# Kernel optimization log

Measured on AMD Instinct MI355X. Metric: run time of the kernel, lower is better.

## Reference

```python
import jax, jax.numpy as jnp
import numpy as np

N = 8192      # total nodes
B = 64        # graphs in batch
NPG = 128     # nodes per graph (equal-size graphs; idx sorted)
D_IN = 256
H = 256       # hidden_dim (d_model)
NH = 4        # nhead
HD = H // NH
FF = 2 * H    # dim_feedforward
NC = 16       # n_class


def setup_inputs() -> dict:
    key = jax.random.key(0)
    ks = jax.random.split(key, 16)
    def rn(k, shp, scale=0.05):
        return jax.random.normal(k, shp, jnp.float32) * scale
    inp = {}
    inp["x_in"] = jax.random.normal(ks[0], (N, D_IN), jnp.float32)
    # scale adjacency so each row sums ~1 to keep activations well-conditioned
    inp["adj"] = jax.random.uniform(ks[1], (N, N), jnp.float32) * (2.0 / N)
    inp["idx"] = jnp.repeat(jnp.arange(B, dtype=jnp.int32), NPG)
    inp["cum_nodes"] = jnp.full((B,), NPG, jnp.int32)
    # fc1
    inp["W1"] = rn(ks[2], (D_IN, H)); inp["b1"] = jnp.zeros((H,), jnp.float32)
    # transformer encoder layer (eval mode, dropout inactive)
    inp["in_w"] = rn(ks[3], (H, 3 * H)); inp["in_b"] = jnp.zeros((3 * H,), jnp.float32)
    inp["out_w"] = rn(ks[4], (H, H));    inp["out_b"] = jnp.zeros((H,), jnp.float32)
    inp["ln1_s"] = jnp.ones((H,), jnp.float32); inp["ln1_b"] = jnp.zeros((H,), jnp.float32)
    inp["ff1_w"] = rn(ks[5], (H, FF)); inp["ff1_b"] = jnp.zeros((FF,), jnp.float32)
    inp["ff2_w"] = rn(ks[6], (FF, H)); inp["ff2_b"] = jnp.zeros((H,), jnp.float32)
    inp["ln2_s"] = jnp.ones((H,), jnp.float32); inp["ln2_b"] = jnp.zeros((H,), jnp.float32)
    # fc3 / fc4
    inp["W3"] = rn(ks[7], (H, H));  inp["b3"] = jnp.zeros((H,), jnp.float32)
    inp["W4"] = rn(ks[8], (H, NC)); inp["b4"] = jnp.zeros((NC,), jnp.float32)
    return inp


def _layer_norm(x, s, b):
    mu = x.mean(-1, keepdims=True)
    xc = x - mu
    return xc * jax.lax.rsqrt((xc * xc).mean(-1, keepdims=True) + 1e-5) * s + b


def reference(x_in, adj, idx, cum_nodes, W1, b1, in_w, in_b, out_w, out_b,
              ln1_s, ln1_b, ff1_w, ff1_b, ff2_w, ff2_b, ln2_s, ln2_b,
              W3, b3, W4, b4):
    Bg = cum_nodes.shape[0]
    n = x_in.shape[0] // Bg  # equal-size graphs -> pad_sequence == reshape
    x = x_in @ W1 + b1                      # fc1
    x = jax.nn.relu(adj @ x)                # adjacency message passing
    p = x.reshape(Bg, n, H)                 # pack: idx is sorted, graphs equal size
    # --- TransformerEncoderLayer (post-LN, relu FFN, eval mode) ---
    qkv = p @ in_w + in_b                   # [B, n, 3H]
    q, k, v = jnp.split(qkv, 3, axis=-1)
    q = q.reshape(Bg, n, NH, HD); k = k.reshape(Bg, n, NH, HD); v = v.reshape(Bg, n, NH, HD)
    att = jax.nn.softmax(jnp.einsum('bqhd,bkhd->bhqk', q, k) / np.sqrt(HD), axis=-1)
    o = jnp.einsum('bhqk,bkhd->bqhd', att, v).reshape(Bg, n, H) @ out_w + out_b
    y = _layer_norm(p + o, ln1_s, ln1_b)
    ff = jax.nn.relu(y @ ff1_w + ff1_b) @ ff2_w + ff2_b
    y = _layer_norm(y + ff, ln2_s, ln2_b)
    # --- unpack + scatter-add pooling over graphs ---
    flat = y.reshape(Bg * n, H)
    pooled = jax.ops.segment_sum(flat, idx, num_segments=Bg)  # [B, H]
    out = jax.nn.relu(pooled @ W3 + b3) @ W4 + b4
    return jax.nn.log_softmax(out, axis=-1)
```

## Files before the change

kernel.cpp:

```cpp
#include <hip/hip_runtime.h>

typedef float fx4 __attribute__((ext_vector_type(4)));
typedef short s16x8 __attribute__((ext_vector_type(8)));
typedef short s16x4 __attribute__((ext_vector_type(4)));
typedef unsigned short ushort_t;

__device__ __forceinline__ short f2bf(float f) {
  union { float f; unsigned u; } v; v.f = f;
  unsigned r = v.u + 0x7FFFu + ((v.u >> 16) & 1u);
  return (short)(r >> 16);
}

__device__ __forceinline__ float bf2f(short h) {
  union { float f; unsigned u; } v;
  v.u = ((unsigned)(unsigned short)h) << 16;
  return v.f;
}

__device__ __forceinline__ unsigned cvt_pk_bf16(float a, float b) {
  unsigned r;
  asm("v_cvt_pk_bf16_f32 %0, %1, %2" : "=v"(r) : "v"(a), "v"(b));
  return r;
}

__device__ __forceinline__ s16x8 cvt8(fx4 a, fx4 b) {
  union { s16x8 s; unsigned u[4]; } w;
  w.u[0] = cvt_pk_bf16(a[0], a[1]);
  w.u[1] = cvt_pk_bf16(a[2], a[3]);
  w.u[2] = cvt_pk_bf16(b[0], b[1]);
  w.u[3] = cvt_pk_bf16(b[2], b[3]);
  return w.s;
}

__device__ __forceinline__ void gload16(const void* g, void* l) {
  __builtin_amdgcn_global_load_lds(
      (const __attribute__((address_space(1))) unsigned int*)g,
      (__attribute__((address_space(3))) unsigned int*)l, 16, 0, 0);
}

__global__ __launch_bounds__(256) void prep_kernel(
    const float* __restrict__ W1, const float* __restrict__ in_w,
    const float* __restrict__ out_w, const float* __restrict__ ff1_w,
    const float* __restrict__ ff2_w,
    ushort_t* __restrict__ W1t, ushort_t* __restrict__ in_wT,
    ushort_t* __restrict__ out_wT, ushort_t* __restrict__ ff1t,
    ushort_t* __restrict__ ff2t) {
  const int bid = blockIdx.x, t = threadIdx.x;
  const float* W; ushort_t* Wt; int K, N, base;
  if (bid < 256)       { W = W1;    Wt = W1t;    K = 256; N = 256; base = 0; }
  else if (bid < 1024) { W = in_w;  Wt = in_wT;  K = 256; N = 768; base = 256; }
  else if (bid < 1280) { W = out_w; Wt = out_wT; K = 256; N = 256; base = 1024; }
  else if (bid < 1792) { W = ff1_w; Wt = ff1t;   K = 256; N = 512; base = 1280; }
  else                 { W = ff2_w; Wt = ff2t;   K = 512; N = 256; base = 1792; }
  const int idx = (bid - base) * 256 + t;
  const int k = idx / N, n = idx - k * N;
  Wt[(size_t)n * K + k] = (ushort_t)f2bf(W[idx]);
}

template<int MF, bool AF32, int OUTM, bool RELU, bool RES>
__global__ __launch_bounds__(256) void gemm2(
    const void* __restrict__ Av, const ushort_t* __restrict__ Bt,
    const float* __restrict__ bias, const float* __restrict__ res,
    const float* __restrict__ lns, const float* __restrict__ lnb,
    float* __restrict__ Cf, ushort_t* __restrict__ Cb,
    int M, int N, int K, int kLen) {
  constexpr int BM = MF * 16;
  __shared__ __align__(16) ushort_t Asm[2][BM * 64];
  __shared__ __align__(16) ushort_t Bsm[256 * 64];
  const int t = threadIdx.x, lane = t & 63, wave = t >> 6;
  const int bm = blockIdx.y * BM;
  const int bn = blockIdx.x * 256;
  const int wn = wave * 64, fr = lane & 15, fq = lane >> 4;
  const int NT = kLen >> 6;
  const int x0 = ((fq) ^ (fr & 7)) * 8;
  const int x1 = ((4 + fq) ^ (fr & 7)) * 8;
  fx4 acc[MF][4] = {};

  const int gl = lane >> 3, gc = lane & 7;
  const int gsw = (gc ^ gl) * 8;
  const ushort_t* Bgl = Bt + (size_t)(bn + wave * 64 + gl) * K + gsw;
  const ushort_t* Agl =
      (const ushort_t*)Av + (size_t)(bm + wave * (BM / 4) + gl) * K + gsw;
  constexpr int TPR = 256 / BM;
  const int arow = t / TPR;
  const int ac0 = (t % TPR) * (BM / 4);
  const float* Afp = (const float*)Av + (size_t)(bm + arow) * K + ac0;
  fx4 R[MF / 2][2];

  auto issueB = [&](int kt) {
    #pragma unroll
    for (int i = 0; i < 8; ++i)
      gload16(Bgl + (size_t)i * 8 * K + kt * 64, &Bsm[wave * 4096 + i * 512]);
  };
  auto issueAg = [&](int buf, int kt) {
    #pragma unroll
    for (int i = 0; i < MF / 2; ++i)
      gload16(Agl + (size_t)i * 8 * K + kt * 64,
              &Asm[buf][wave * (BM * 16) + i * 512]);
  };
  auto loadR = [&](int kt) {
    #pragma unroll
    for (int w = 0; w < MF / 2; ++w) {
      R[w][0] = *(const fx4*)(Afp + kt * 64 + w * 8);
      R[w][1] = *(const fx4*)(Afp + kt * 64 + w * 8 + 4);
    }
  };
  auto writeA = [&](int buf) {
    #pragma unroll
    for (int w = 0; w < MF / 2; ++w) {
      const int cs = ((ac0 >> 3) + w) ^ (arow & 7);
      *(s16x8*)&Asm[buf][arow * 64 + cs * 8] = cvt8(R[w][0], R[w][1]);
    }
  };

  if constexpr (AF32) { loadR(0); issueB(0); writeA(0); loadR(1); }
  else { issueAg(0, 0); issueB(0); }
  __syncthreads();

  #pragma unroll 1
  for (int kt = 0; kt < NT; ++kt) {
    const int cur = kt & 1;
    s16x8 b0[4], b1[4], a0[MF], a1[MF];
    #pragma unroll
    for (int nf = 0; nf < 4; ++nf) {
      b0[nf] = *(const s16x8*)&Bsm[(wn + nf * 16 + fr) * 64 + x0];
      b1[nf] = *(const s16x8*)&Bsm[(wn + nf * 16 + fr) * 64 + x1];
    }
    #pragma unroll
    for (int mf = 0; mf < MF; ++mf)
      a0[mf] = *(const s16x8*)&Asm[cur][(mf * 16 + fr) * 64 + x0];
    asm volatile("s_waitcnt lgkmcnt(0)" ::: "memory");
    if (kt + 1 < NT) {
      if constexpr (AF32) {
        writeA(cur ^ 1);
        if (kt + 2 < NT) loadR(kt + 2);
        issueB(kt + 1);
      } else {
        issueAg(cur ^ 1, kt + 1);
        issueB(kt + 1);
      }
    }
    #pragma unroll
    for (int mf = 0; mf < MF; ++mf)
      #pragma unroll
      for (int nf = 0; nf < 4; ++nf)
        acc[mf][nf] = __builtin_amdgcn_mfma_f32_16x16x32_bf16(
            a0[mf], b0[nf], acc[mf][nf], 0, 0, 0);
    #pragma unroll
    for (int mf = 0; mf < MF; ++mf)
      a1[mf] = *(const s16x8*)&Asm[cur][(mf * 16 + fr) * 64 + x1];
    #pragma unroll
    for (int mf = 0; mf < MF; ++mf)
      #pragma unroll
      for (int nf = 0; nf < 4; ++nf)
        acc[mf][nf] = __builtin_amdgcn_mfma_f32_16x16x32_bf16(
            a1[mf], b1[nf], acc[mf][nf], 0, 0, 0);
    __syncthreads();
  }

  if constexpr (OUTM == 3) {
    #pragma unroll
    for (int mf = 0; mf < MF; ++mf)
      #pragma unroll
      for (int nf = 0; nf < 4; ++nf) {
        const int col = bn + wn + nf * 16 + fr;
        const float bb = bias[col];
        s16x4 w;
        #pragma unroll
        for (int r = 0; r < 4; ++r) w[r] = f2bf(acc[mf][nf][r] + bb);
        *(s16x4*)&Cb[(size_t)col * M + bm + mf * 16 + fq * 4] = w;
      }
  } else {
    #pragma unroll
    for (int mf = 0; mf < MF; ++mf)
      #pragma unroll
      for (int nf = 0; nf < 4; ++nf) {
        const int col = bn + wn + nf * 16 + fr;
        const float bb = bias[col];
        #pragma unroll
        for (int r = 0; r < 4; ++r) {
          const int row = bm + mf * 16 + fq * 4 + r;
          float x = acc[mf][nf][r] + bb;
          if constexpr (RES) x += res[(size_t)row * N + col];
          if constexpr (RELU) x = fmaxf(x, 0.f);
          if constexpr (OUTM == 0 || OUTM == 2) Cf[(size_t)row * N + col] = x;
          if constexpr (OUTM == 1 || OUTM == 2)
            Cb[(size_t)row * N + col] = (ushort_t)f2bf(x);
        }
      }
  }
}

__global__ __launch_bounds__(256) void adjmm2(
    const float* __restrict__ adj, const ushort_t* __restrict__ xT,
    ushort_t* __restrict__ part) {
  constexpr int NT = 32;
  __shared__ __align__(16) ushort_t Asm[2][64 * 64];
  __shared__ __align__(16) ushort_t Bsm[2][256 * 64];
  const int t = threadIdx.x, lane = t & 63, wave = t >> 6;
  const int kh = blockIdx.x, bm = blockIdx.y * 64;
  const int kOff = kh * 2048;
  const int wn = wave * 64, fr = lane & 15, fq = lane >> 4;
  const int x0 = (fq ^ (fr & 7)) * 8, x1 = ((4 + fq) ^ (fr & 7)) * 8;
  const int gl = lane >> 3, gc = lane & 7, gsw = (gc ^ gl) * 8;

  const ushort_t* Bgl = xT + (size_t)(wn + gl) * 8192 + kOff + gsw;
  const int arow = t >> 2;
  const int ac0 = (t & 3) * 16;
  const float* Afp = adj + (size_t)(bm + arow) * 8192 + kOff + ac0;

  fx4 R[2][2];
  auto loadR = [&](int kt) {
    #pragma unroll
    for (int w = 0; w < 2; ++w) {
      R[w][0] = *(const fx4*)(Afp + kt * 64 + w * 8);
      R[w][1] = *(const fx4*)(Afp + kt * 64 + w * 8 + 4);
    }
  };
  auto writeA = [&](int buf) {
    #pragma unroll
    for (int w = 0; w < 2; ++w) {
      const int cs = ((ac0 >> 3) + w) ^ (arow & 7);
      *(s16x8*)&Asm[buf][arow * 64 + cs * 8] = cvt8(R[w][0], R[w][1]);
    }
  };
  auto issueB = [&](int buf, int kt) {
    #pragma unroll
    for (int i = 0; i < 8; ++i)
      gload16(Bgl + (size_t)i * 8 * 8192 + kt * 64,
              &Bsm[buf][wave * 4096 + i * 512]);
  };

  fx4 acc[4][4] = {};
  loadR(0);
  issueB(0, 0);
  writeA(0);
  loadR(1);
  asm volatile("s_waitcnt lgkmcnt(0)" ::: "memory");
  asm volatile("s_waitcnt vmcnt(4)" ::: "memory");
  __builtin_amdgcn_sched_barrier(0);
  __builtin_amdgcn_s_barrier();
  __builtin_amdgcn_sched_barrier(0);
  issueB(1, 1);

  #pragma unroll 1
  for (int kt = 0; kt < NT; ++kt) {
    const int cur = kt & 1;
    s16x8 a0[4], a1[4], b0[4], b1[4];
    #pragma unroll
    for (int mf = 0; mf < 4; ++mf) {
      a0[mf] = *(const s16x8*)&Asm[cur][(mf * 16 + fr) * 64 + x0];
      a1[mf] = *(const s16x8*)&Asm[cur][(mf * 16 + fr) * 64 + x1];
    }
    #pragma unroll
    for (int nf = 0; nf < 4; ++nf) {
      b0[nf] = *(const s16x8*)&Bsm[cur][(wn + nf * 16 + fr) * 64 + x0];
      b1[nf] = *(const s16x8*)&Bsm[cur][(wn + nf * 16 + fr) * 64 + x1];
    }
    if (kt + 1 < NT) {
      writeA(cur ^ 1);
      if (kt + 2 < NT) loadR(kt + 2);
    }
    #pragma unroll
    for (int mf = 0; mf < 4; ++mf)
      #pragma unroll
      for (int nf = 0; nf < 4; ++nf)
        acc[mf][nf] = __builtin_amdgcn_mfma_f32_16x16x32_bf16(
            a0[mf], b0[nf], acc[mf][nf], 0, 0, 0);
    #pragma unroll
    for (int mf = 0; mf < 4; ++mf)
      #pragma unroll
      for (int nf = 0; nf < 4; ++nf)
        acc[mf][nf] = __builtin_amdgcn_mfma_f32_16x16x32_bf16(
            a1[mf], b1[nf], acc[mf][nf], 0, 0, 0);
    asm volatile("s_waitcnt lgkmcnt(0)" ::: "memory");
    if (kt + 2 < NT)
      asm volatile("s_waitcnt vmcnt(4)" ::: "memory");
    else
      asm volatile("s_waitcnt vmcnt(0)" ::: "memory");
    __builtin_amdgcn_sched_barrier(0);
    __builtin_amdgcn_s_barrier();
    __builtin_amdgcn_sched_barrier(0);
    if (kt + 2 < NT) issueB(cur, kt + 2);
  }

  ushort_t* po = part + (size_t)kh * (8192ull * 256ull);
  #pragma unroll
  for (int mf = 0; mf < 4; ++mf)
    #pragma unroll
    for (int nf = 0; nf < 4; ++nf)
      #pragma unroll
      for (int r = 0; r < 4; ++r)
        po[(size_t)(bm + mf * 16 + fq * 4 + r) * 256 + wn + nf * 16 + fr] =
            (ushort_t)f2bf(acc[mf][nf][r]);
}

__global__ __launch_bounds__(256) void relu_reduce4(
    const ushort_t* __restrict__ part, float* __restrict__ p,
    ushort_t* __restrict__ pb) {
  const size_t i = ((size_t)blockIdx.x * 256 + threadIdx.x) * 8;
  const size_t S = 8192ull * 256ull;
  float a[8] = {};
  #pragma unroll
  for (int j = 0; j < 4; ++j) {
    const s16x8 v = *(const s16x8*)(part + j * S + i);
    #pragma unroll
    for (int c = 0; c < 8; ++c) a[c] += bf2f(v[c]);
  }
  fx4 v0, v1;
  #pragma unroll
  for (int c = 0; c < 4; ++c) {
    v0[c] = fmaxf(a[c], 0.f);
    v1[c] = fmaxf(a[c + 4], 0.f);
  }
  *(fx4*)(p + i) = v0;
  *(fx4*)(p + i + 4) = v1;
  s16x8 w;
  #pragma unroll
  for (int c = 0; c < 4; ++c) { w[c] = f2bf(v0[c]); w[c + 4] = f2bf(v1[c]); }
  *(s16x8*)(pb + i) = w;
}

__global__ __launch_bounds__(256) void att_fused(
    const ushort_t* __restrict__ qkv, ushort_t* __restrict__ attout) {
  __shared__ float k_s[128][68];
  __shared__ float v_s[128][68];
  __shared__ float s_s[128][129];
  __shared__ float pm[2][128];
  __shared__ float ps[2][128];
  const int bh = blockIdx.x, b = bh >> 2, h = bh & 3;
  const int t = threadIdx.x;
  const ushort_t* qb = qkv + (size_t)b * 128 * 768 + h * 64;
  for (int u = t; u < 1024; u += 256) {
    const int n = u >> 3, d8 = (u & 7) * 8;
    const s16x8 kk = *(const s16x8*)(qb + (size_t)n * 768 + 256 + d8);
    const s16x8 vv = *(const s16x8*)(qb + (size_t)n * 768 + 512 + d8);
    #pragma unroll
    for (int c = 0; c < 8; ++c) {
      k_s[n][d8 + c] = bf2f(kk[c]);
      v_s[n][d8 + c] = bf2f(vv[c]);
    }
  }
  const int row = t & 127, kh = t >> 7;
  fx4 qr[16];
  {
    const s16x8* q8 = (const s16x8*)(qb + (size_t)row * 768);
    #pragma unroll
    for (int j = 0; j < 8; ++j) {
      const s16x8 qv = q8[j];
      qr[2*j][0] = bf2f(qv[0]); qr[2*j][1] = bf2f(qv[1]);
      qr[2*j][2] = bf2f(qv[2]); qr[2*j][3] = bf2f(qv[3]);
      qr[2*j+1][0] = bf2f(qv[4]); qr[2*j+1][1] = bf2f(qv[5]);
      qr[2*j+1][2] = bf2f(qv[6]); qr[2*j+1][3] = bf2f(qv[7]);
    }
  }
  __syncthreads();
  float m = -1e30f;
  for (int j = 0; j < 64; ++j) {
    const int jj = kh * 64 + j;
    const fx4* kr = (const fx4*)&k_s[jj][0];
    float s0 = 0.f, s1 = 0.f, s2 = 0.f, s3 = 0.f;
    #pragma unroll
    for (int c = 0; c < 16; c += 4) {
      fx4 k0 = kr[c], k1 = kr[c + 1], k2 = kr[c + 2], k3 = kr[c + 3];
      s0 += qr[c][0]*k0[0] + qr[c][1]*k0[1] + qr[c][2]*k0[2] + qr[c][3]*k0[3];
      s1 += qr[c+1][0]*k1[0] + qr[c+1][1]*k1[1] + qr[c+1][2]*k1[2] + qr[c+1][3]*k1[3];
      s2 += qr[c+2][0]*k2[0] + qr[c+2][1]*k2[1] + qr[c+2][2]*k2[2] + qr[c+2][3]*k2[3];
      s3 += qr[c+3][0]*k3[0] + qr[c+3][1]*k3[1] + qr[c+3][2]*k3[2] + qr[c+3][3]*k3[3];
    }
    const float s = (s0 + s1 + s2 + s3) * 0.125f;
    s_s[row][jj] = s;
    m = fmaxf(m, s);
  }
  pm[kh][row] = m;
  __syncthreads();
  const float m2 = fmaxf(pm[0][row], pm[1][row]);
  float sum = 0.f;
  for (int j = 0; j < 64; ++j) {
    const int jj = kh * 64 + j;
    const float e = __expf(s_s[row][jj] - m2);
    s_s[row][jj] = e;
    sum += e;
  }
  ps[kh][row] = sum;
  __syncthreads();
  const int row2 = t >> 1, dh = (t & 1) * 32;
  const float inv = 1.f / (ps[0][row2] + ps[1][row2]);
  fx4 acc4[8] = {};
  for (int k = 0; k < 128; ++k) {
    const float e = s_s[row2][k];
    const fx4* vr = (const fx4*)&v_s[k][dh];
    #pragma unroll
    for (int c = 0; c < 8; ++c) acc4[c] += e * vr[c];
  }
  ushort_t* orow = attout + (size_t)(b * 128 + row2) * 256 + h * 64 + dh;
  #pragma unroll
  for (int c = 0; c < 8; ++c) {
    const fx4 v = acc4[c] * inv;
    s16x4 w;
    #pragma unroll
    for (int j = 0; j < 4; ++j) w[j] = f2bf(v[j]);
    *(s16x4*)(orow + c * 4) = w;
  }
}

__global__ __launch_bounds__(256) void tail_kernel(
    const ushort_t* __restrict__ attout, const ushort_t* __restrict__ out_wT,
    const float* __restrict__ out_b, const float* __restrict__ p_res,
    const float* __restrict__ ln1_s, const float* __restrict__ ln1_b,
    const ushort_t* __restrict__ ff1t, const float* __restrict__ ff1_b,
    const ushort_t* __restrict__ ff2t, const float* __restrict__ ff2_b,
    const float* __restrict__ ln2_s, const float* __restrict__ ln2_b,
    float* __restrict__ pooled4) {
  __shared__ __align__(16) ushort_t Asm[2][32 * 64];
  __shared__ __align__(16) ushort_t Bsm[256 * 64];
  __shared__ __align__(16) ushort_t y_s[32 * 256];
  __shared__ __align__(16) ushort_t f1_s[32 * 512];
  __shared__ float red_s[128], red_q[128];
  const int t = threadIdx.x, lane = t & 63, wave = t >> 6;
  const int bq = blockIdx.x, bm = bq * 32;
  const int wn = wave * 64, fr = lane & 15, fq = lane >> 4;
  const int x0 = (fq ^ (fr & 7)) * 8, x1 = ((4 + fq) ^ (fr & 7)) * 8;
  const int gl = lane >> 3, gc = lane & 7, gsw = (gc ^ gl) * 8;

  fx4 acc[2][4] = {};
  {
    const ushort_t* Agl = attout + (size_t)(bm + wave * 8 + gl) * 256 + gsw;
    const ushort_t* Bgl = out_wT + (size_t)(wave * 64 + gl) * 256 + gsw;
    auto issueA = [&](int buf, int kt) {
      gload16(Agl + kt * 64, &Asm[buf][wave * 512]);
    };
    auto issueB = [&](int kt) {
      #pragma unroll
      for (int i = 0; i < 8; ++i)
        gload16(Bgl + (size_t)i * 8 * 256 + kt * 64,
                &Bsm[wave * 4096 + i * 512]);
    };
    issueA(0, 0); issueB(0);
    __syncthreads();
    #pragma unroll 1
    for (int kt = 0; kt < 4; ++kt) {
      const int cur = kt & 1;
      s16x8 b0[4], b1[4], a0[2], a1[2];
      #pragma unroll
      for (int nf = 0; nf < 4; ++nf) {
        b0[nf] = *(const s16x8*)&Bsm[(wn + nf * 16 + fr) * 64 + x0];
        b1[nf] = *(const s16x8*)&Bsm[(wn + nf * 16 + fr) * 64 + x1];
      }
      #pragma unroll
      for (int mf = 0; mf < 2; ++mf) {
        a0[mf] = *(const s16x8*)&Asm[cur][(mf * 16 + fr) * 64 + x0];
        a1[mf] = *(const s16x8*)&Asm[cur][(mf * 16 + fr) * 64 + x1];
      }
      asm volatile("s_waitcnt lgkmcnt(0)" ::: "memory");
      if (kt < 3) { issueA(cur ^ 1, kt + 1); issueB(kt + 1); }
      #pragma unroll
      for (int mf = 0; mf < 2; ++mf)
        #pragma unroll
        for (int nf = 0; nf < 4; ++nf) {
          acc[mf][nf] = __builtin_amdgcn_mfma_f32_16x16x32_bf16(
              a0[mf], b0[nf], acc[mf][nf], 0, 0, 0);
          acc[mf][nf] = __builtin_amdgcn_mfma_f32_16x16x32_bf16(
              a1[mf], b1[nf], acc[mf][nf], 0, 0, 0);
        }
      __syncthreads();
    }
  }
  float yv[2][4][4];
  #pragma unroll
  for (int mf = 0; mf < 2; ++mf)
    #pragma unroll
    for (int nf = 0; nf < 4; ++nf) {
      const int col = wn + nf * 16 + fr;
      #pragma unroll
      for (int r = 0; r < 4; ++r) {
        const int row = bm + mf * 16 + fq * 4 + r;
        yv[mf][nf][r] = acc[mf][nf][r] + out_b[col] +
                        p_res[(size_t)row * 256 + col];
      }
    }
  {
    #pragma unroll
    for (int mf = 0; mf < 2; ++mf)
      #pragma unroll
      for (int r = 0; r < 4; ++r) {
        float s = yv[mf][0][r] + yv[mf][1][r] + yv[mf][2][r] + yv[mf][3][r];
        float q = yv[mf][0][r]*yv[mf][0][r] + yv[mf][1][r]*yv[mf][1][r] +
                  yv[mf][2][r]*yv[mf][2][r] + yv[mf][3][r]*yv[mf][3][r];
        #pragma unroll
        for (int off = 1; off < 16; off <<= 1) {
          s += __shfl_xor(s, off, 64);
          q += __shfl_xor(q, off, 64);
        }
        if (fr == 0) {
          red_s[(mf * 16 + fq * 4 + r) * 4 + wave] = s;
          red_q[(mf * 16 + fq * 4 + r) * 4 + wave] = q;
        }
      }
    __syncthreads();
    #pragma unroll
    for (int mf = 0; mf < 2; ++mf)
      #pragma unroll
      for (int r = 0; r < 4; ++r) {
        const int rl = mf * 16 + fq * 4 + r;
        const float st = red_s[rl*4] + red_s[rl*4+1] + red_s[rl*4+2] + red_s[rl*4+3];
        const float qt = red_q[rl*4] + red_q[rl*4+1] + red_q[rl*4+2] + red_q[rl*4+3];
        const float mu = st * (1.f / 256.f);
        const float rr = rsqrtf(qt * (1.f / 256.f) - mu * mu + 1e-5f);
        #pragma unroll
        for (int nf = 0; nf < 4; ++nf) {
          const int col = wn + nf * 16 + fr;
          const float o = (yv[mf][nf][r] - mu) * rr * ln1_s[col] + ln1_b[col];
          yv[mf][nf][r] = o;
          y_s[rl * 256 + ((col >> 3) ^ (rl & 7)) * 8 + (col & 7)] =
              (ushort_t)f2bf(o);
        }
      }
  }
  __syncthreads();

  #pragma unroll 1
  for (int ng = 0; ng < 2; ++ng) {
    const ushort_t* Bgl = ff1t + (size_t)(ng * 256 + wave * 64 + gl) * 256 + gsw;
    auto issueB = [&](int kt) {
      #pragma unroll
      for (int i = 0; i < 8; ++i)
        gload16(Bgl + (size_t)i * 8 * 256 + kt * 64,
                &Bsm[wave * 4096 + i * 512]);
    };
    fx4 a2[2][4] = {};
    issueB(0);
    #pragma unroll 1
    for (int kt = 0; kt < 4; ++kt) {
      asm volatile("s_waitcnt vmcnt(0)" ::: "memory");
      s16x8 b0[4], b1[4], a0[2], a1[2];
      #pragma unroll
      for (int nf = 0; nf < 4; ++nf) {
        b0[nf] = *(const s16x8*)&Bsm[(wn + nf * 16 + fr) * 64 + x0];
        b1[nf] = *(const s16x8*)&Bsm[(wn + nf * 16 + fr) * 64 + x1];
      }
      #pragma unroll
      for (int mf = 0; mf < 2; ++mf) {
        const int row = mf * 16 + fr;
        a0[mf] = *(const s16x8*)&y_s[row * 256 + ((kt*8 + fq) ^ (row & 7)) * 8];
        a1[mf] = *(const s16x8*)&y_s[row * 256 + ((kt*8 + 4 + fq) ^ (row & 7)) * 8];
      }
      asm volatile("s_waitcnt lgkmcnt(0)" ::: "memory");
      if (kt < 3) issueB(kt + 1);
      #pragma unroll
      for (int mf = 0; mf < 2; ++mf)
        #pragma unroll
        for (int nf = 0; nf < 4; ++nf) {
          a2[mf][nf] = __builtin_amdgcn_mfma_f32_16x16x32_bf16(
              a0[mf], b0[nf], a2[mf][nf], 0, 0, 0);
          a2[mf][nf] = __builtin_amdgcn_mfma_f32_16x16x32_bf16(
              a1[mf], b1[nf], a2[mf][nf], 0, 0, 0);
        }
    }
    #pragma unroll
    for (int mf = 0; mf < 2; ++mf)
      #pragma unroll
      for (int nf = 0; nf < 4; ++nf) {
        const int col = ng * 256 + wn + nf * 16 + fr;
        const float bb = ff1_b[col];
        #pragma unroll
        for (int r = 0; r < 4; ++r) {
          const int rl = mf * 16 + fq * 4 + r;
          const float x = fmaxf(a2[mf][nf][r] + bb, 0.f);
          f1_s[rl * 512 + ((col >> 3) ^ (rl & 7)) * 8 + (col & 7)] =
              (ushort_t)f2bf(x);
        }
      }
  }
  __syncthreads();

  {
    const ushort_t* Bgl = ff2t + (size_t)(wave * 64 + gl) * 512 + gsw;
    auto issueB = [&](int kt) {
      #pragma unroll
      for (int i = 0; i < 8; ++i)
        gload16(Bgl + (size_t)i * 8 * 512 + kt * 64,
                &Bsm[wave * 4096 + i * 512]);
    };
    fx4 a3[2][4] = {};
    issueB(0);
    #pragma unroll 1
    for (int kt = 0; kt < 8; ++kt) {
      asm volatile("s_waitcnt vmcnt(0)" ::: "memory");
      s16x8 b0[4], b1[4], a0[2], a1[2];
      #pragma unroll
      for (int nf = 0; nf < 4; ++nf) {
        b0[nf] = *(const s16x8*)&Bsm[(wn + nf * 16 + fr) * 64 + x0];
        b1[nf] = *(const s16x8*)&Bsm[(wn + nf * 16 + fr) * 64 + x1];
      }
      #pragma unroll
      for (int mf = 0; mf < 2; ++mf) {
        const int row = mf * 16 + fr;
        a0[mf] = *(const s16x8*)&f1_s[row * 512 + ((kt*8 + fq) ^ (row & 7)) * 8];
        a1[mf] = *(const s16x8*)&f1_s[row * 512 + ((kt*8 + 4 + fq) ^ (row & 7)) * 8];
      }
      asm volatile("s_waitcnt lgkmcnt(0)" ::: "memory");
      if (kt < 7) issueB(kt + 1);
      #pragma unroll
      for (int mf = 0; mf < 2; ++mf)
        #pragma unroll
        for (int nf = 0; nf < 4; ++nf) {
          a3[mf][nf] = __builtin_amdgcn_mfma_f32_16x16x32_bf16(
              a0[mf], b0[nf], a3[mf][nf], 0, 0, 0);
          a3[mf][nf] = __builtin_amdgcn_mfma_f32_16x16x32_bf16(
              a1[mf], b1[nf], a3[mf][nf], 0, 0, 0);
        }
    }
    float vv[2][4][4];
    #pragma unroll
    for (int mf = 0; mf < 2; ++mf)
      #pragma unroll
      for (int nf = 0; nf < 4; ++nf) {
        const int col = wn + nf * 16 + fr;
        const float bb = ff2_b[col];
        #pragma unroll
        for (int r = 0; r < 4; ++r)
          vv[mf][nf][r] = a3[mf][nf][r] + bb + yv[mf][nf][r];
      }
    __syncthreads();
    #pragma unroll
    for (int mf = 0; mf < 2; ++mf)
      #pragma unroll
      for (int r = 0; r < 4; ++r) {
        float s = vv[mf][0][r] + vv[mf][1][r] + vv[mf][2][r] + vv[mf][3][r];
        float q = vv[mf][0][r]*vv[mf][0][r] + vv[mf][1][r]*vv[mf][1][r] +
                  vv[mf][2][r]*vv[mf][2][r] + vv[mf][3][r]*vv[mf][3][r];
        #pragma unroll
        for (int off = 1; off < 16; off <<= 1) {
          s += __shfl_xor(s, off, 64);
          q += __shfl_xor(q, off, 64);
        }
        if (fr == 0) {
          red_s[(mf * 16 + fq * 4 + r) * 4 + wave] = s;
          red_q[(mf * 16 + fq * 4 + r) * 4 + wave] = q;
        }
      }
    __syncthreads();
    float colsum[4] = {};
    #pragma unroll
    for (int mf = 0; mf < 2; ++mf)
      #pragma unroll
      for (int r = 0; r < 4; ++r) {
        const int rl = mf * 16 + fq * 4 + r;
        const float st = red_s[rl*4] + red_s[rl*4+1] + red_s[rl*4+2] + red_s[rl*4+3];
        const float qt = red_q[rl*4] + red_q[rl*4+1] + red_q[rl*4+2] + red_q[rl*4+3];
        const float mu = st * (1.f / 256.f);
        const float rr = rsqrtf(qt * (1.f / 256.f) - mu * mu + 1e-5f);
        #pragma unroll
        for (int nf = 0; nf < 4; ++nf) {
          const int col = wn + nf * 16 + fr;
          colsum[nf] += (vv[mf][nf][r] - mu) * rr * ln2_s[col] + ln2_b[col];
        }
      }
    #pragma unroll
    for (int nf = 0; nf < 4; ++nf) {
      colsum[nf] += __shfl_xor(colsum[nf], 16, 64);
      colsum[nf] += __shfl_xor(colsum[nf], 32, 64);
    }
    if (lane < 16)
      #pragma unroll
      for (int nf = 0; nf < 4; ++nf)
        pooled4[(size_t)bq * 256 + wn + nf * 16 + fr] = colsum[nf];
  }
}

__global__ __launch_bounds__(256) void head_kernel(
    const float* __restrict__ pooled4, const float* __restrict__ W3,
    const float* __restrict__ b3, const float* __restrict__ W4,
    const float* __restrict__ b4, float* __restrict__ out) {
  __shared__ float sp[256];
  __shared__ float t1[256];
  __shared__ float logits[16];
  const int b = blockIdx.x, h = threadIdx.x;
  sp[h] = pooled4[(size_t)(b * 4 + 0) * 256 + h] +
          pooled4[(size_t)(b * 4 + 1) * 256 + h] +
          pooled4[(size_t)(b * 4 + 2) * 256 + h] +
          pooled4[(size_t)(b * 4 + 3) * 256 + h];
  __syncthreads();
  float a = b3[h];
  for (int k = 0; k < 256; ++k) a += sp[k] * W3[k * 256 + h];
  t1[h] = fmaxf(a, 0.f);
  __syncthreads();
  if (h < 16) {
    float o = b4[h];
    for (int j = 0; j < 256; ++j) o += t1[j] * W4[j * 16 + h];
    logits[h] = o;
  }
  __syncthreads();
  if (h < 16) {
    float mm = -1e30f;
    #pragma unroll
    for (int c = 0; c < 16; ++c) mm = fmaxf(mm, logits[c]);
    float se = 0.f;
    #pragma unroll
    for (int c = 0; c < 16; ++c) se += __expf(logits[c] - mm);
    out[b * 16 + h] = logits[h] - mm - logf(se);
  }
}

extern "C" void kernel_launch(void* const* d_in, const int* in_sizes, int n_in,
                              void* d_out, int out_size, void* d_ws, size_t ws_size,
                              hipStream_t stream) {
  const float* x_in  = (const float*)d_in[0];
  const float* adj   = (const float*)d_in[1];
  const float* W1    = (const float*)d_in[4];
  const float* b1    = (const float*)d_in[5];
  const float* in_w  = (const float*)d_in[6];
  const float* in_b  = (const float*)d_in[7];
  const float* out_w = (const float*)d_in[8];
  const float* out_b = (const float*)d_in[9];
  const float* ln1_s = (const float*)d_in[10];
  const float* ln1_b = (const float*)d_in[11];
  const float* ff1_w = (const float*)d_in[12];
  const float* ff1_b = (const float*)d_in[13];
  const float* ff2_w = (const float*)d_in[14];
  const float* ff2_b = (const float*)d_in[15];
  const float* ln2_s = (const float*)d_in[16];
  const float* ln2_b = (const float*)d_in[17];
  const float* W3    = (const float*)d_in[18];
  const float* b3    = (const float*)d_in[19];
  const float* W4    = (const float*)d_in[20];
  const float* b4    = (const float*)d_in[21];
  char* ws = (char*)d_ws;
  const size_t MB = 1ull << 20;
  ushort_t* xT      = (ushort_t*)(ws);
  ushort_t* W1t     = (ushort_t*)(ws + 4 * MB);
  ushort_t* in_wT   = (ushort_t*)(ws + 4 * MB + 131072);
  ushort_t* out_wT  = (ushort_t*)(ws + 4 * MB + 524288);
  ushort_t* ff1t    = (ushort_t*)(ws + 4 * MB + 655360);
  ushort_t* ff2t    = (ushort_t*)(ws + 4 * MB + 917504);
  float*    p       = (float*)(ws + 8 * MB);
  ushort_t* p_bf    = (ushort_t*)(ws + 16 * MB);
  ushort_t* qkv_bf  = (ushort_t*)(ws + 20 * MB);
  ushort_t* attout  = (ushort_t*)(ws + 32 * MB);
  float*    pooled4 = (float*)(ws + 36 * MB);
  ushort_t* part    = (ushort_t*)(ws + 37 * MB);
  float*    outp    = (float*)d_out;
  (void)in_sizes; (void)n_in; (void)out_size; (void)ws_size;

  prep_kernel<<<2304, 256, 0, stream>>>(W1, in_w, out_w, ff1_w, ff2_w,
                                        W1t, in_wT, out_wT, ff1t, ff2t);
  gemm2<2, true, 3, false, false><<<dim3(1, 256), 256, 0, stream>>>(
      x_in, W1t, b1, nullptr, nullptr, nullptr, nullptr, xT,
      8192, 256, 256, 256);
  adjmm2<<<dim3(4, 128), 256, 0, stream>>>(adj, xT, part);
  relu_reduce4<<<1024, 256, 0, stream>>>(part, p, p_bf);
  gemm2<4, false, 1, false, false><<<dim3(3, 128), 256, 0, stream>>>(
      p_bf, in_wT, in_b, nullptr, nullptr, nullptr, nullptr, qkv_bf,
      8192, 768, 256, 256);
  att_fused<<<256, 256, 0, stream>>>(qkv_bf, attout);
  tail_kernel<<<256, 256, 0, stream>>>(
      attout, out_wT, out_b, p, ln1_s, ln1_b, ff1t, ff1_b,
      ff2t, ff2_b, ln2_s, ln2_b, pooled4);
  head_kernel<<<64, 256, 0, stream>>>(pooled4, W3, b3, W4, b4, outp);
}
```

Before: 183.3 us.

## Load adjacency tiles straight into MFMA fragment registers, drop A LDS staging

The adjacency GEMM kernel now has each wave load fp32 adjacency rows from global memory straight into registers laid out as MFMA fragments, converting them to bf16 in place. This removes the A shared-memory double buffer and its write/read round trip. The B tile uses a single wave-private LDS buffer, so per-iteration block barriers become a barrier every fourth step. In exchange, every wave loads the full 64-row A tile, so A is fetched four times per block and relies on the caches, with less coalesced access patterns.

Result: slower. 259.9 us (+41.8%).

```diff
diff --git a/kernel.cpp b/kernel.cpp
--- a/kernel.cpp
+++ b/kernel.cpp
@@ -191,97 +191,73 @@
   }
 }
 
-__global__ __launch_bounds__(256) void adjmm2(
+__global__ __launch_bounds__(256) void adjmm3(
     const float* __restrict__ adj, const ushort_t* __restrict__ xT,
     ushort_t* __restrict__ part) {
   constexpr int NT = 32;
-  __shared__ __align__(16) ushort_t Asm[2][64 * 64];
-  __shared__ __align__(16) ushort_t Bsm[2][256 * 64];
+  __shared__ __align__(16) ushort_t Bsm[256 * 64];
   const int t = threadIdx.x, lane = t & 63, wave = t >> 6;
   const int kh = blockIdx.x, bm = blockIdx.y * 64;
   const int kOff = kh * 2048;
   const int wn = wave * 64, fr = lane & 15, fq = lane >> 4;
   const int x0 = (fq ^ (fr & 7)) * 8, x1 = ((4 + fq) ^ (fr & 7)) * 8;
-  const int gl = lane >> 3, gc = lane & 7, gsw = (gc ^ gl) * 8;
+  const int gl = lane >> 3, gsw = ((lane & 7) ^ gl) * 8;
 
   const ushort_t* Bgl = xT + (size_t)(wn + gl) * 8192 + kOff + gsw;
-  const int arow = t >> 2;
-  const int ac0 = (t & 3) * 16;
-  const float* Afp = adj + (size_t)(bm + arow) * 8192 + kOff + ac0;
-
-  fx4 R[2][2];
+  const float* Ag = adj + (size_t)(bm + fr) * 8192 + kOff + fq * 8;
+
+  fx4 R[4][2][2];
   auto loadR = [&](int kt) {
     #pragma unroll
-    for (int w = 0; w < 2; ++w) {
-      R[w][0] = *(const fx4*)(Afp + kt * 64 + w * 8);
-      R[w][1] = *(const fx4*)(Afp + kt * 64 + w * 8 + 4);
-    }
+    for (int mf = 0; mf < 4; ++mf)
+      #pragma unroll
+      for (int kk = 0; kk < 2; ++kk) {
+        const float* ap = Ag + (size_t)mf * 16 * 8192 + kt * 64 + kk * 32;
+        R[mf][kk][0] = *(const fx4*)ap;
+        R[mf][kk][1] = *(const fx4*)(ap + 4);
+      }
   };
-  auto writeA = [&](int buf) {
-    #pragma unroll
-    for (int w = 0; w < 2; ++w) {
-      const int cs = ((ac0 >> 3) + w) ^ (arow & 7);
-      *(s16x8*)&Asm[buf][arow * 64 + cs * 8] = cvt8(R[w][0], R[w][1]);
-    }
-  };
-  auto issueB = [&](int buf, int kt) {
+  auto issueB = [&](int kt) {
     #pragma unroll
     for (int i = 0; i < 8; ++i)
       gload16(Bgl + (size_t)i * 8 * 8192 + kt * 64,
-              &Bsm[buf][wave * 4096 + i * 512]);
+              &Bsm[wave * 4096 + i * 512]);
   };
 
   fx4 acc[4][4] = {};
+  issueB(0);
   loadR(0);
-  issueB(0, 0);
-  writeA(0);
-  loadR(1);
-  asm volatile("s_waitcnt lgkmcnt(0)" ::: "memory");
-  asm volatile("s_waitcnt vmcnt(4)" ::: "memory");
-  __builtin_amdgcn_sched_barrier(0);
-  __builtin_amdgcn_s_barrier();
-  __builtin_amdgcn_sched_barrier(0);
-  issueB(1, 1);
 
   #pragma unroll 1
   for (int kt = 0; kt < NT; ++kt) {
-    const int cur = kt & 1;
-    s16x8 a0[4], a1[4], b0[4], b1[4];
-    #pragma unroll
-    for (int mf = 0; mf < 4; ++mf) {
-      a0[mf] = *(const s16x8*)&Asm[cur][(mf * 16 + fr) * 64 + x0];
-      a1[mf] = *(const s16x8*)&Asm[cur][(mf * 16 + fr) * 64 + x1];
-    }
+    asm volatile("s_waitcnt vmcnt(16)" ::: "memory");
+    __builtin_amdgcn_sched_barrier(0);
+    s16x8 b0[4], b1[4];
     #pragma unroll
     for (int nf = 0; nf < 4; ++nf) {
-      b0[nf] = *(const s16x8*)&Bsm[cur][(wn + nf * 16 + fr) * 64 + x0];
-      b1[nf] = *(const s16x8*)&Bsm[cur][(wn + nf * 16 + fr) * 64 + x1];
-    }
-    if (kt + 1 < NT) {
-      writeA(cur ^ 1);
-      if (kt + 2 < NT) loadR(kt + 2);
-    }
+      b0[nf] = *(const s16x8*)&Bsm[(wn + nf * 16 + fr) * 64 + x0];
+      b1[nf] = *(const s16x8*)&Bsm[(wn + nf * 16 + fr) * 64 + x1];
+    }
+    asm volatile("s_waitcnt lgkmcnt(0)" ::: "memory");
+    __builtin_amdgcn_sched_barrier(0);
+    if (kt + 1 < NT) issueB(kt + 1);
+    s16x8 af[4][2];
     #pragma unroll
     for (int mf = 0; mf < 4; ++mf)
       #pragma unroll
-      for (int nf = 0; nf < 4; ++nf)
-        acc[mf][nf] = __builtin_amdgcn_mfma_f32_16x16x32_bf16(
-            a0[mf], b0[nf], acc[mf][nf], 0, 0, 0);
-    #pragma unroll
-    for (int mf = 0; mf < 4; ++mf)
-      #pragma unroll
-      for (int nf = 0; nf < 4; ++nf)
-        acc[mf][nf] = __builtin_amdgcn_mfma_f32_16x16x32_bf16(
-            a1[mf], b1[nf], acc[mf][nf], 0, 0, 0);
-    asm volatile("s_waitcnt lgkmcnt(0)" ::: "memory");
-    if (kt + 2 < NT)
-      asm volatile("s_waitcnt vmcnt(4)" ::: "memory");
-    else
-      asm volatile("s_waitcnt vmcnt(0)" ::: "memory");
-    __builtin_amdgcn_sched_barrier(0);
-    __builtin_amdgcn_s_barrier();
-    __builtin_amdgcn_sched_barrier(0);
-    if (kt + 2 < NT) issueB(cur, kt + 2);
+      for (int kk = 0; kk < 2; ++kk)
+        af[mf][kk] = cvt8(R[mf][kk][0], R[mf][kk][1]);
+    if (kt + 1 < NT) loadR(kt + 1);
+    #pragma unroll
+    for (int kk = 0; kk < 2; ++kk) {
+      #pragma unroll
+      for (int mf = 0; mf < 4; ++mf)
+        #pragma unroll
+        for (int nf = 0; nf < 4; ++nf)
+          acc[mf][nf] = __builtin_amdgcn_mfma_f32_16x16x32_bf16(
+              af[mf][kk], kk ? b1[nf] : b0[nf], acc[mf][nf], 0, 0, 0);
+    }
+    if ((kt & 3) == 3) __builtin_amdgcn_s_barrier();
   }
 
   ushort_t* po = part + (size_t)kh * (8192ull * 256ull);
@@ -748,7 +724,7 @@
   gemm2<2, true, 3, false, false><<<dim3(1, 256), 256, 0, stream>>>(
       x_in, W1t, b1, nullptr, nullptr, nullptr, nullptr, xT,
       8192, 256, 256, 256);
-  adjmm2<<<dim3(4, 128), 256, 0, stream>>>(adj, xT, part);
+  adjmm3<<<dim3(4, 128), 256, 0, stream>>>(adj, xT, part);
   relu_reduce4<<<1024, 256, 0, stream>>>(part, p, p_bf);
   gemm2<4, false, 1, false, false><<<dim3(3, 128), 256, 0, stream>>>(
       p_bf, in_wT, in_b, nullptr, nullptr, nullptr, nullptr, qkv_bf,
```
